# Optimization experiments

Hardware: AMD Instinct MI355X
Metric: run time of the kernel (lower is better)

The kernel has to match this reference:

```python
import jax, jax.numpy as jnp
import numpy as np


def setup_inputs() -> dict:
    key = jax.random.key(0)
    k1, k2 = jax.random.split(key)
    logits = jax.random.normal(k1, (4, 19, 512, 512), dtype=jnp.float32)
    targets = jax.random.randint(k2, (4, 512, 512), 0, 19, dtype=jnp.int64)
    return {"logits": logits, "targets": targets}


def reference(logits, targets):
    # Lovasz-Softmax loss, classes='all', per_image=False, ignore=None.
    B, C, H, W = logits.shape
    probs = jax.nn.softmax(logits, axis=1)                    # [B,C,H,W]
    p = probs.transpose(0, 2, 3, 1).reshape(-1, C)            # [P,C], P=B*H*W
    t = targets.reshape(-1)                                   # [P]
    fg = jax.nn.one_hot(t, C, dtype=p.dtype).T                # [C,P]
    errors = jnp.abs(fg - p.T)                                # [C,P]
    # sort errors descending per class, carry ground-truth along
    perm = jnp.argsort(-errors, axis=1)                       # [C,P]
    errors_sorted = jnp.take_along_axis(errors, perm, axis=1)
    gt_sorted = jnp.take_along_axis(fg, perm, axis=1)
    # Lovasz extension gradient (vectorized over classes)
    gts = gt_sorted.sum(axis=1, keepdims=True)                # [C,1]
    cs = jnp.cumsum(gt_sorted, axis=1)                        # [C,P]
    intersection = gts - cs
    union = gts + jnp.cumsum(1.0 - gt_sorted, axis=1)
    jaccard = 1.0 - intersection / union
    jaccard = jnp.concatenate(
        [jaccard[:, :1], jaccard[:, 1:] - jaccard[:, :-1]], axis=1)
    losses = jnp.sum(errors_sorted * jaccard, axis=1)         # [C]
    return jnp.mean(losses)
```

## Files before the change

### kernel.cpp

```cpp
#include <hip/hip_runtime.h>

constexpr int C    = 19;
constexpr int HW   = 512 * 512;
constexpr int NP   = 4 * HW;
constexpr int NB   = 256;
constexpr int NBLK = 1024;
constexpr int TPB  = 1024;
constexpr int CHUNKS = 16;

__global__ __launch_bounds__(TPB, 8) void lovasz_hist(
    const float* __restrict__ logits,
    const int*   __restrict__ targets,
    unsigned int* __restrict__ partials)
{
    __shared__ unsigned int hist[C * NB];
    const int tid = threadIdx.x;

    for (int i = tid; i < C * NB; i += TPB) hist[i] = 0;
    __syncthreads();

    const int pix = blockIdx.x * TPB + tid;
    const int b   = pix >> 18;
    const int hw  = pix & (HW - 1);
    const float* lp = logits + (size_t)b * (C * HW) + hw;

    float l[C];
    float s = 0.f;
#pragma unroll
    for (int c = 0; c < C; ++c) {
        float ex = __expf(lp[(size_t)c * HW]);
        l[c] = ex;
        s += ex;
    }
    const float inv = 1.0f / s;
    const int   t   = targets[pix];

#pragma unroll
    for (int c = 0; c < C; ++c) {
        float p  = l[c] * inv;
        bool  fg = (c == t);
        float e  = fg ? 1.0f - p : p;
        int bin = (int)(__fsqrt_rn(e) * (float)NB);
        bin = bin > NB - 1 ? NB - 1 : bin;
        atomicAdd(&hist[c * NB + bin], fg ? 0x10001u : 1u);
    }

    __syncthreads();
    unsigned int* dst = partials + (size_t)blockIdx.x * (C * NB);
    for (int i = tid; i < C * NB; i += TPB) dst[i] = hist[i];
}

__global__ __launch_bounds__(256) void lovasz_reduce(
    const unsigned int* __restrict__ partials,
    unsigned long long* __restrict__ lvl2,
    float* __restrict__ out)
{
    if (blockIdx.x == 0 && threadIdx.x == 0) out[0] = 0.f;

    const int c   = blockIdx.x / CHUNKS;
    const int ch  = blockIdx.x % CHUNKS;
    const int bin = threadIdx.x;
    const int kpc = NBLK / CHUNKS;

    unsigned long long acc = 0;
    for (int k = ch * kpc; k < (ch + 1) * kpc; ++k) {
        unsigned v = partials[(size_t)k * (C * NB) + c * NB + bin];
        acc += (unsigned long long)(v & 0xFFFFu) |
               ((unsigned long long)(v >> 16) << 32);
    }
    lvl2[((size_t)c * CHUNKS + ch) * NB + bin] = acc;
}

__global__ __launch_bounds__(256) void lovasz_loss(
    const unsigned long long* __restrict__ lvl2,
    float* __restrict__ out)
{
    const int c   = blockIdx.x;
    const int tid = threadIdx.x;

    __shared__ unsigned long long red[256];

    unsigned long long acc = 0;
#pragma unroll
    for (int ch = 0; ch < CHUNKS; ++ch)
        acc += lvl2[((size_t)c * CHUNKS + ch) * NB + tid];

    red[tid] = acc;
    __syncthreads();
    for (int off = 128; off > 0; off >>= 1) {
        if (tid < off) red[tid] += red[tid + off];
        __syncthreads();
    }
    const float G = (float)(unsigned)(red[0] >> 32);
    __syncthreads();

    const int bin = NB - 1 - tid;
    const unsigned long long v = acc;
    red[tid] = v;
    __syncthreads();
    unsigned long long x = red[NB - 1 - tid];
    __syncthreads();
    red[tid] = x;
    __syncthreads();
    const unsigned long long mine = x;
    for (int off = 1; off < 256; off <<= 1) {
        unsigned long long y = (tid >= off) ? red[tid - off] : 0ull;
        __syncthreads();
        x += y;
        red[tid] = x;
        __syncthreads();
    }

    const unsigned long long after  = x;
    const unsigned long long before = after - mine;
    float loss = 0.f;
    if ((unsigned)mine) {
        float Ka  = (float)(unsigned)(after);
        float CSa = (float)(unsigned)(after >> 32);
        float Kb  = (float)(unsigned)(before);
        float CSb = (float)(unsigned)(before >> 32);
        float Ja = (Ka > 0.f) ? 1.f - (G - CSa) / (G + Ka - CSa) : 0.f;
        float Jb = (Kb > 0.f) ? 1.f - (G - CSb) / (G + Kb - CSb) : 0.f;
        float r  = ((float)bin + 0.5f) * (1.0f / (float)NB);
        loss = (r * r) * (Ja - Jb);
    }

    __shared__ float sf[256];
    sf[tid] = loss;
    __syncthreads();
    for (int off = 128; off > 0; off >>= 1) {
        if (tid < off) sf[tid] += sf[tid + off];
        __syncthreads();
    }
    if (tid == 0) atomicAdd(out, sf[0] * (1.0f / (float)C));
}

extern "C" void kernel_launch(void* const* d_in, const int* in_sizes, int n_in,
                              void* d_out, int out_size, void* d_ws, size_t ws_size,
                              hipStream_t stream) {
    const float* logits  = (const float*)d_in[0];
    const int*   targets = (const int*)d_in[1];
    float*       out     = (float*)d_out;

    unsigned int*       partials = (unsigned int*)d_ws;
    unsigned long long* lvl2     = (unsigned long long*)
        ((char*)d_ws + (size_t)NBLK * C * NB * sizeof(unsigned int));

    lovasz_hist<<<NBLK, TPB, 0, stream>>>(logits, targets, partials);
    lovasz_reduce<<<C * CHUNKS, 256, 0, stream>>>(partials, lvl2, out);
    lovasz_loss<<<C, 256, 0, stream>>>(lvl2, out);
}
```

Baseline: 129.3 us.

## Process two pixels per thread and fuse reduce and loss kernels into one

The histogram kernel now handles two pixels per thread with half as many blocks, which halves the per-block partial histograms written to and read back from global memory. The separate chunked reduce and loss kernels are merged into one 1024-thread-per-class kernel that sums all partials, scans and computes the loss. This removes a launch and the intermediate lvl2 buffer. In exchange only 19 blocks now read 512 partials each, which may limit parallelism in the final reduction. The output zeroing moves into the histogram kernel.

```diff
diff --git a/kernel.cpp b/kernel.cpp
--- a/kernel.cpp
+++ b/kernel.cpp
@@ -4,45 +4,51 @@
 constexpr int HW   = 512 * 512;
 constexpr int NP   = 4 * HW;
 constexpr int NB   = 256;
-constexpr int NBLK = 1024;
+constexpr int NBLK = 512;
 constexpr int TPB  = 1024;
-constexpr int CHUNKS = 16;
+constexpr int PPT  = 2;
 
 __global__ __launch_bounds__(TPB, 8) void lovasz_hist(
     const float* __restrict__ logits,
     const int*   __restrict__ targets,
-    unsigned int* __restrict__ partials)
+    unsigned int* __restrict__ partials,
+    float* __restrict__ out)
 {
     __shared__ unsigned int hist[C * NB];
     const int tid = threadIdx.x;
 
+    if (blockIdx.x == 0 && tid == 0) out[0] = 0.f;
+
     for (int i = tid; i < C * NB; i += TPB) hist[i] = 0;
     __syncthreads();
 
-    const int pix = blockIdx.x * TPB + tid;
-    const int b   = pix >> 18;
-    const int hw  = pix & (HW - 1);
-    const float* lp = logits + (size_t)b * (C * HW) + hw;
+#pragma unroll
+    for (int j = 0; j < PPT; ++j) {
+        const int pix = blockIdx.x * (TPB * PPT) + j * TPB + tid;
+        const int b   = pix >> 18;
+        const int hw  = pix & (HW - 1);
+        const float* lp = logits + (size_t)b * (C * HW) + hw;
 
-    float l[C];
-    float s = 0.f;
+        float l[C];
+        float s = 0.f;
 #pragma unroll
-    for (int c = 0; c < C; ++c) {
-        float ex = __expf(lp[(size_t)c * HW]);
-        l[c] = ex;
-        s += ex;
-    }
-    const float inv = 1.0f / s;
-    const int   t   = targets[pix];
+        for (int c = 0; c < C; ++c) {
+            float ex = __expf(lp[(size_t)c * HW]);
+            l[c] = ex;
+            s += ex;
+        }
+        const float inv = 1.0f / s;
+        const int   t   = targets[pix];
 
 #pragma unroll
-    for (int c = 0; c < C; ++c) {
-        float p  = l[c] * inv;
-        bool  fg = (c == t);
-        float e  = fg ? 1.0f - p : p;
-        int bin = (int)(__fsqrt_rn(e) * (float)NB);
-        bin = bin > NB - 1 ? NB - 1 : bin;
-        atomicAdd(&hist[c * NB + bin], fg ? 0x10001u : 1u);
+        for (int c = 0; c < C; ++c) {
+            float p  = l[c] * inv;
+            bool  fg = (c == t);
+            float e  = fg ? 1.0f - p : p;
+            int bin = (int)(__fsqrt_rn(e) * (float)NB);
+            bin = bin > NB - 1 ? NB - 1 : bin;
+            atomicAdd(&hist[c * NB + bin], fg ? 0x10001u : 1u);
+        }
     }
 
     __syncthreads();
@@ -50,85 +56,73 @@
     for (int i = tid; i < C * NB; i += TPB) dst[i] = hist[i];
 }
 
-__global__ __launch_bounds__(256) void lovasz_reduce(
+__global__ __launch_bounds__(1024) void lovasz_final(
     const unsigned int* __restrict__ partials,
-    unsigned long long* __restrict__ lvl2,
     float* __restrict__ out)
 {
-    if (blockIdx.x == 0 && threadIdx.x == 0) out[0] = 0.f;
+    const int c   = blockIdx.x;
+    const int tid = threadIdx.x;
+    const int bin = tid & (NB - 1);
+    const int kg  = tid >> 8;
+    constexpr int KPG = NBLK / 4;
 
-    const int c   = blockIdx.x / CHUNKS;
-    const int ch  = blockIdx.x % CHUNKS;
-    const int bin = threadIdx.x;
-    const int kpc = NBLK / CHUNKS;
+    __shared__ unsigned long long sm[1024];
 
     unsigned long long acc = 0;
-    for (int k = ch * kpc; k < (ch + 1) * kpc; ++k) {
+    for (int k = kg * KPG; k < (kg + 1) * KPG; ++k) {
         unsigned v = partials[(size_t)k * (C * NB) + c * NB + bin];
         acc += (unsigned long long)(v & 0xFFFFu) |
                ((unsigned long long)(v >> 16) << 32);
     }
-    lvl2[((size_t)c * CHUNKS + ch) * NB + bin] = acc;
-}
+    sm[tid] = acc;
+    __syncthreads();
 
-__global__ __launch_bounds__(256) void lovasz_loss(
-    const unsigned long long* __restrict__ lvl2,
-    float* __restrict__ out)
-{
-    const int c   = blockIdx.x;
-    const int tid = threadIdx.x;
+    unsigned long long binsum = 0;
+    if (tid < NB)
+        binsum = sm[bin] + sm[bin + 256] + sm[bin + 512] + sm[bin + 768];
+    __syncthreads();
 
-    __shared__ unsigned long long red[256];
-
-    unsigned long long acc = 0;
-#pragma unroll
-    for (int ch = 0; ch < CHUNKS; ++ch)
-        acc += lvl2[((size_t)c * CHUNKS + ch) * NB + tid];
-
-    red[tid] = acc;
+    if (tid < NB) sm[tid] = binsum;
     __syncthreads();
     for (int off = 128; off > 0; off >>= 1) {
-        if (tid < off) red[tid] += red[tid + off];
+        if (tid < off) sm[tid] += sm[tid + off];
         __syncthreads();
     }
-    const float G = (float)(unsigned)(red[0] >> 32);
+    const float G = (float)(unsigned)(sm[0] >> 32);
     __syncthreads();
 
-    const int bin = NB - 1 - tid;
-    const unsigned long long v = acc;
-    red[tid] = v;
+    if (tid < NB) sm[tid] = binsum;
     __syncthreads();
-    unsigned long long x = red[NB - 1 - tid];
+    unsigned long long mine = (tid < NB) ? sm[NB - 1 - tid] : 0ull;
     __syncthreads();
-    red[tid] = x;
+    if (tid < NB) sm[tid] = mine;
     __syncthreads();
-    const unsigned long long mine = x;
-    for (int off = 1; off < 256; off <<= 1) {
-        unsigned long long y = (tid >= off) ? red[tid - off] : 0ull;
+    unsigned long long x = mine;
+    for (int off = 1; off < NB; off <<= 1) {
+        unsigned long long y = (tid >= off && tid < NB) ? sm[tid - off] : 0ull;
         __syncthreads();
-        x += y;
-        red[tid] = x;
+        if (tid < NB) { x += y; sm[tid] = x; }
         __syncthreads();
     }
 
-    const unsigned long long after  = x;
-    const unsigned long long before = after - mine;
     float loss = 0.f;
-    if ((unsigned)mine) {
+    if (tid < NB && (unsigned)mine) {
+        const unsigned long long after  = x;
+        const unsigned long long before = after - mine;
         float Ka  = (float)(unsigned)(after);
         float CSa = (float)(unsigned)(after >> 32);
         float Kb  = (float)(unsigned)(before);
         float CSb = (float)(unsigned)(before >> 32);
         float Ja = (Ka > 0.f) ? 1.f - (G - CSa) / (G + Ka - CSa) : 0.f;
         float Jb = (Kb > 0.f) ? 1.f - (G - CSb) / (G + Kb - CSb) : 0.f;
-        float r  = ((float)bin + 0.5f) * (1.0f / (float)NB);
+        float r  = ((float)(NB - 1 - tid) + 0.5f) * (1.0f / (float)NB);
         loss = (r * r) * (Ja - Jb);
     }
 
-    __shared__ float sf[256];
+    __shared__ float sf[1024];
     sf[tid] = loss;
     __syncthreads();
-    for (int off = 128; off > 0; off >>= 1) {
+    for (int off = 512; off > 0; off >>= 1) {
         if (tid < off) sf[tid] += sf[tid + off];
         __syncthreads();
     }
@@ -141,12 +135,8 @@
     const float* logits  = (const float*)d_in[0];
     const int*   targets = (const int*)d_in[1];
     float*       out     = (float*)d_out;
+    unsigned int* partials = (unsigned int*)d_ws;
 
-    unsigned int*       partials = (unsigned int*)d_ws;
-    unsigned long long* lvl2     = (unsigned long long*)
-        ((char*)d_ws + (size_t)NBLK * C * NB * sizeof(unsigned int));
-
-    lovasz_hist<<<NBLK, TPB, 0, stream>>>(logits, targets, partials);
-    lovasz_reduce<<<C * CHUNKS, 256, 0, stream>>>(partials, lvl2, out);
-    lovasz_loss<<<C, 256, 0, stream>>>(lvl2, out);
+    lovasz_hist<<<NBLK, TPB, 0, stream>>>(logits, targets, partials, out);
+    lovasz_final<<<C, 1024, 0, stream>>>(partials, out);
 }
```

Result: slower. 156.6 us (+21.1%).
